# Optimization experiments

Hardware: AMD Instinct MI355X
Metric: run time of the kernel (lower is better)

The kernel has to match this reference:

```python
import jax, jax.numpy as jnp
import numpy as np
from math import sqrt

B, L, S, H, E = 4, 2048, 2048, 8, 64
T = 1.0  # softmax temperature


def setup_inputs() -> dict:
    key = jax.random.key(0)
    kq, kk, kv = jax.random.split(key, 3)
    q = jax.random.normal(kq, (B, L, H, E), dtype=jnp.float32)
    k = jax.random.normal(kk, (B, S, H, E), dtype=jnp.float32)
    v = jax.random.normal(kv, (B, S, H, E), dtype=jnp.float32)
    mask = jnp.zeros((B, L), dtype=jnp.bool_)  # unused by the module, kept for signature fidelity
    return {"q": q, "k": k, "v": v, "mask": mask}


def reference(q, k, v, mask):
    Bq, Lq, Hq, Eq = q.shape
    # [B,L,H,E] -> [B,H,E,L]; FFT over time axis
    xq = jnp.transpose(q, (0, 2, 3, 1))
    xk = jnp.transpose(k, (0, 2, 3, 1))
    xv = jnpp_t = jnp.transpose(v, (0, 2, 3, 1))
    xq_ft = jnp.fft.rfft(xq, axis=-1, norm='ortho')   # [B,H,E,Lf]
    xk_ft = jnp.fft.rfft(xk, axis=-1, norm='ortho')   # [B,H,E,Sf]
    xv_ft = jnp.fft.rfft(xv, axis=-1, norm='ortho')   # [B,H,E,Sf]
    # complex frequency-domain scores [B,H,Lf,Sf]
    scores = jnp.einsum('bhex,bhey->bhxy', xq_ft, jnp.conj(xk_ft)) / sqrt(Eq)
    # activation == 'softmax': softmax over |scores|/T, then real-weighted complex mix
    attn = jax.nn.softmax(jnp.abs(scores) / T, axis=-1)
    xqkv_ft = jnp.einsum('bhxy,bhey->bhex', attn.astype(xv_ft.dtype), xv_ft)  # [B,H,E,Lf]
    out = jnp.fft.irfft(xqkv_ft, n=Lq, axis=-1, norm='ortho')  # [B,H,E,L]
    return jnp.transpose(out, (0, 3, 1, 2))  # [B,L,H,E]
```

## Files before the change

kernel.cpp:

```cpp
#include <hip/hip_runtime.h>
#include <hip/hip_bf16.h>
#include <math.h>

#define LOGN  11
#define NN    2048
#define LOGM  10
#define MM    1024
#define NF    1025
#define NYP   1056
#define TWO_PI 6.283185307179586f
#define INV_SQRT_N 0.022097086912079608f
#define INV_SCALE  0.044194173824159216f

typedef __attribute__((ext_vector_type(8))) short bhalf8;
typedef __attribute__((ext_vector_type(4))) float f32x4;

#define MFMA16(a, b, c) __builtin_amdgcn_mfma_f32_16x16x32_bf16(a, b, c, 0, 0, 0)

__device__ __forceinline__ unsigned short f2bf(float f) {
    union { float f; unsigned u; } v; v.f = f;
    unsigned r = v.u + 0x7FFFu + ((v.u >> 16) & 1u);
    return (unsigned short)(r >> 16);
}
__device__ __forceinline__ float bf2f(unsigned short h) {
    union { unsigned u; float f; } v; v.u = ((unsigned)h) << 16;
    return v.f;
}

__device__ __forceinline__ void fft_stages_m(float2* buf, const float2* tw, int tid)
{
    for (int st = 1; st <= LOGM; st++) {
        int half = 1 << (st - 1);
        #pragma unroll
        for (int it = 0; it < 2; it++) {
            int j   = tid + 256 * it;
            int pos = j & (half - 1);
            int grp = j >> (st - 1);
            int i0  = (grp << st) + pos;
            int i1  = i0 + half;
            float2 w = tw[pos << (LOGM - st)];
            float2 a = buf[i0];
            float2 b = buf[i1];
            float2 bw = make_float2(b.x * w.x - b.y * w.y,
                                    b.x * w.y + b.y * w.x);
            buf[i0] = make_float2(a.x + bw.x, a.y + bw.y);
            buf[i1] = make_float2(a.x - bw.x, a.y - bw.y);
        }
        __syncthreads();
    }
}

__global__ __launch_bounds__(256) void tr_fwd(const float* __restrict__ q,
                                              const float* __restrict__ k,
                                              const float* __restrict__ v,
                                              unsigned short* __restrict__ ttr)
{
    __shared__ float Ts[64][65];
    int tt     = blockIdx.x;
    int h      = blockIdx.y;
    int z      = blockIdx.z;
    int tensor = z >> 2;
    int b      = z & 3;
    int tid    = threadIdx.x;
    int t0     = tt * 64;

    const float* in = (tensor == 0) ? q : (tensor == 1) ? k : v;

    {
        int tl = tid >> 2, ec = (tid & 3) * 16;
        const float* src = in + ((size_t)b * 2048 + t0 + tl) * 512 + h * 64 + ec;
        #pragma unroll
        for (int m = 0; m < 4; m++) {
            float4 v4 = *(const float4*)(src + m * 4);
            Ts[tl][ec + m * 4 + 0] = v4.x;
            Ts[tl][ec + m * 4 + 1] = v4.y;
            Ts[tl][ec + m * 4 + 2] = v4.z;
            Ts[tl][ec + m * 4 + 3] = v4.w;
        }
    }
    __syncthreads();
    {
        int el = tid >> 2, tc = (tid & 3) * 16;
        size_t row = ((size_t)(tensor * 32 + b * 8 + h)) * 64 + el;
        unsigned short* dst = ttr + row * 2048 + t0 + tc;
        #pragma unroll
        for (int j = 0; j < 16; j++) dst[j] = f2bf(Ts[tc + j][el]);
    }
}

__global__ __launch_bounds__(256) void fft_fwd(const unsigned short* __restrict__ ttr,
                                               unsigned short* __restrict__ Pq,
                                               unsigned short* __restrict__ Pk,
                                               unsigned short* __restrict__ Pv)
{
    __shared__ float2 buf[MM];
    __shared__ float2 tw[MM / 2];

    int g      = blockIdx.x;
    int p      = g % 96;
    int e      = g / 96;
    int tensor = p / 32;
    int bh     = p % 32;
    int tid    = threadIdx.x;

    unsigned short* plane = (tensor == 0) ? Pq : (tensor == 1) ? Pk : Pv;

    for (int i = tid; i < MM / 2; i += 256) {
        float ang = -TWO_PI * (float)i / (float)MM;
        float sv, cv;
        __sincosf(ang, &sv, &cv);
        tw[i] = make_float2(cv, sv);
    }

    const unsigned short* src = ttr + ((size_t)p * 64 + e) * 2048;
    #pragma unroll
    for (int i = 0; i < 4; i++) {
        int j = tid + 256 * i;
        unsigned pr = *(const unsigned*)(src + 2 * j);
        float x0 = bf2f((unsigned short)(pr & 0xFFFFu));
        float x1 = bf2f((unsigned short)(pr >> 16));
        buf[__brev((unsigned)j) >> (32 - LOGM)] = make_float2(x0, x1);
    }
    __syncthreads();

    fft_stages_m(buf, tw, tid);

    unsigned short* dre = plane + ((size_t)bh * 128 + e) * NYP;
    unsigned short* dim_ = dre + (size_t)64 * NYP;

    for (int kk = tid; kk < NF; kk += 256) {
        float2 A  = buf[kk & (MM - 1)];
        float2 Bc = buf[(MM - kk) & (MM - 1)];
        float Ex = 0.5f * (A.x + Bc.x), Ey = 0.5f * (A.y - Bc.y);
        float Dx = 0.5f * (A.x - Bc.x), Dy = 0.5f * (A.y + Bc.y);
        float Ox = Dy, Oy = -Dx;
        float th = -(TWO_PI / (float)NN) * (float)kk;
        float sn, cs;
        __sincosf(th, &sn, &cs);
        float Xr = Ex + cs * Ox - sn * Oy;
        float Xi = Ey + cs * Oy + sn * Ox;
        dre[kk]  = f2bf(Xr * INV_SQRT_N);
        dim_[kk] = f2bf(Xi * INV_SQRT_N);
    }
    for (int y = NF + tid; y < NYP; y += 256) { dre[y] = 0; dim_[y] = 0; }
}

__global__ __launch_bounds__(256) void qkpack(const unsigned short* __restrict__ Pq,
                                              const unsigned short* __restrict__ Pk,
                                              unsigned short* __restrict__ Qp,
                                              unsigned short* __restrict__ Kp)
{
    __shared__ unsigned short Ts[32][136];
    int y0  = blockIdx.x * 32;
    int bh  = blockIdx.y;
    int tsr = blockIdx.z;
    int tid = threadIdx.x;

    const unsigned short* srcp = (tsr == 0) ? Pq : Pk;
    unsigned short* dstp       = (tsr == 0) ? Qp : Kp;

    {
        int kk = tid >> 1, seg = tid & 1;
        const unsigned short* sp = srcp + ((size_t)bh * 128 + kk) * NYP + y0 + seg * 16;
        #pragma unroll
        for (int j = 0; j < 16; j++) Ts[seg * 16 + j][kk] = sp[j];
    }
    __syncthreads();
    {
        int y = tid >> 3, c = tid & 7;
        unsigned short* dst = dstp + ((size_t)bh * NYP + y0 + y) * 128 + c * 16;
        #pragma unroll
        for (int j = 0; j < 16; j++) dst[j] = Ts[y][c * 16 + j];
    }
}

struct FlashShared {
    union {
        struct {
            unsigned short Ks[32][136];
            unsigned short Vs[128][40];
        } kv;
        unsigned short OutT[128][72];
    } u;
    unsigned short Ps[4][16][40];
};

__global__ __launch_bounds__(256) void flash_mfma(
    const unsigned short* __restrict__ Qp,
    const unsigned short* __restrict__ Kp,
    const unsigned short* __restrict__ Vt,
    unsigned short* __restrict__ numb,
    float* __restrict__ lbuf)
{
    __shared__ FlashShared S;

    int g    = blockIdx.x;
    int bh   = g & 31;
    int idx  = g >> 5;
    int half = idx / 17;
    int x0   = (idx % 17) * 64;
    int tid  = threadIdx.x;
    int w    = tid >> 6;
    int lane = tid & 63;
    int qd   = lane >> 4;
    int col  = lane & 15;

    int xrow = x0 + w * 16 + col;
    int xq   = min(xrow, 1024);
    const unsigned short* qb = Qp + ((size_t)bh * NYP + xq) * 128 + qd * 8;
    bhalf8 Are[4], Aim[4];
    #pragma unroll
    for (int ks = 0; ks < 4; ks++) Are[ks] = *(const bhalf8*)(qb + ks * 32);
    Aim[0] = Are[2];
    Aim[1] = Are[3];
    #pragma unroll
    for (int ks = 0; ks < 2; ks++) {
        bhalf8 t = Are[ks];
        unsigned* u = (unsigned*)&t;
        #pragma unroll
        for (int j = 0; j < 4; j++) u[j] ^= 0x80008000u;
        Aim[ks + 2] = t;
    }

    f32x4 O[8];
    #pragma unroll
    for (int n = 0; n < 8; n++) O[n] = (f32x4){0.f, 0.f, 0.f, 0.f};
    float Lacc[4] = {0.f, 0.f, 0.f, 0.f};

    const unsigned short* kpb = Kp + (size_t)bh * NYP * 128;
    const unsigned short* vtb = Vt + (size_t)bh * 128 * NYP;

    int yy = tid >> 3, c = tid & 7;
    int ee = tid >> 1, h = tid & 1;

    int yt0 = half * 17, yt1 = min(33, yt0 + 17);

    uint4 kc0, kc1, vc0, vc1;
    {
        const uint4* s4 = (const uint4*)(kpb + ((size_t)(yt0 * 32 + yy)) * 128 + c * 16);
        kc0 = s4[0]; kc1 = s4[1];
        const uint4* s5 = (const uint4*)(vtb + (size_t)ee * NYP + yt0 * 32 + h * 16);
        vc0 = s5[0]; vc1 = s5[1];
    }

    for (int yt = yt0; yt < yt1; yt++) {
        __syncthreads();
        *(uint4*)&S.u.kv.Ks[yy][c * 16]     = kc0;
        *(uint4*)&S.u.kv.Ks[yy][c * 16 + 8] = kc1;
        *(uint4*)&S.u.kv.Vs[ee][h * 16]     = vc0;
        *(uint4*)&S.u.kv.Vs[ee][h * 16 + 8] = vc1;
        __syncthreads();

        uint4 kn0, kn1, vn0, vn1;
        if (yt + 1 < yt1) {
            int y0n = (yt + 1) * 32;
            const uint4* s4 = (const uint4*)(kpb + ((size_t)(y0n + yy)) * 128 + c * 16);
            kn0 = s4[0]; kn1 = s4[1];
            const uint4* s5 = (const uint4*)(vtb + (size_t)ee * NYP + y0n + h * 16);
            vn0 = s5[0]; vn1 = s5[1];
        }

        f32x4 sre[2], sim[2];
        #pragma unroll
        for (int sc = 0; sc < 2; sc++) {
            sre[sc] = (f32x4){0.f, 0.f, 0.f, 0.f};
            sim[sc] = (f32x4){0.f, 0.f, 0.f, 0.f};
        }
        #pragma unroll
        for (int sc = 0; sc < 2; sc++)
            #pragma unroll
            for (int ks = 0; ks < 4; ks++) {
                bhalf8 bfrag = *(const bhalf8*)&S.u.kv.Ks[col + 16 * sc][ks * 32 + qd * 8];
                sre[sc] = MFMA16(Are[ks], bfrag, sre[sc]);
                sim[sc] = MFMA16(Aim[ks], bfrag, sim[sc]);
            }

        #pragma unroll
        for (int r = 0; r < 4; r++) {
            float re0 = sre[0][r], im0 = sim[0][r];
            float re1 = sre[1][r], im1 = sim[1][r];
            float p0 = __expf(0.125f * sqrtf(re0 * re0 + im0 * im0));
            float p1 = __expf(0.125f * sqrtf(re1 * re1 + im1 * im1));
            Lacc[r] += p0 + p1;
            S.Ps[w][qd * 4 + r][col]      = f2bf(p0);
            S.Ps[w][qd * 4 + r][col + 16] = f2bf(p1);
        }

        bhalf8 pa = *(const bhalf8*)&S.Ps[w][col][qd * 8];
        #pragma unroll
        for (int n = 0; n < 8; n++) {
            bhalf8 bv = *(const bhalf8*)&S.u.kv.Vs[n * 16 + col][qd * 8];
            O[n] = MFMA16(pa, bv, O[n]);
        }

        kc0 = kn0; kc1 = kn1; vc0 = vn0; vc1 = vn1;
    }

    size_t hofs = (size_t)half * 32 * NYP;
    #pragma unroll
    for (int r = 0; r < 4; r++) {
        float ls = Lacc[r];
        ls += __shfl_xor(ls, 1);
        ls += __shfl_xor(ls, 2);
        ls += __shfl_xor(ls, 4);
        ls += __shfl_xor(ls, 8);
        if (half == 1) ls -= 31.0f;
        int x = x0 + w * 16 + qd * 4 + r;
        if (x <= 1024 && col == 0) lbuf[hofs + (size_t)bh * NYP + x] = ls;
    }

    __syncthreads();
    #pragma unroll
    for (int r = 0; r < 4; r++)
        #pragma unroll
        for (int n = 0; n < 8; n++)
            S.u.OutT[n * 16 + col][w * 16 + qd * 4 + r] = f2bf(O[n][r]);
    __syncthreads();
    {
        int kk2 = tid >> 1, seg = tid & 1;
        int xg  = x0 + seg * 32;
        if (xg < NYP) {
            unsigned short* dst =
                numb + (((size_t)half * 32 + bh) * 128 + kk2) * NYP + xg;
            const unsigned short* srcl = &S.u.OutT[kk2][seg * 32];
            #pragma unroll
            for (int m = 0; m < 4; m++)
                *(uint4*)(dst + m * 8) = *(const uint4*)(srcl + m * 8);
        }
    }
}

__global__ __launch_bounds__(256) void fft_inv(const unsigned short* __restrict__ numb,
                                               const float* __restrict__ lbuf,
                                               float* __restrict__ st)
{
    __shared__ float2 buf[MM];
    __shared__ float2 tw[MM / 2];

    int s   = blockIdx.x;
    int e   = s & 63;
    int bh  = s >> 6;
    int tid = threadIdx.x;

    for (int i = tid; i < MM / 2; i += 256) {
        float ang = TWO_PI * (float)i / (float)MM;
        float sv, cv;
        __sincosf(ang, &sv, &cv);
        tw[i] = make_float2(cv, sv);
    }

    const size_t HS = (size_t)32 * 128 * NYP;
    const unsigned short* nbr = numb + ((size_t)bh * 128 + e) * NYP;
    const unsigned short* nbi = numb + ((size_t)bh * 128 + 64 + e) * NYP;
    const float* l0 = lbuf + (size_t)bh * NYP;
    const float* l1 = l0 + (size_t)32 * NYP;

    #pragma unroll
    for (int i = 0; i < 4; i++) {
        int kk = tid + 256 * i;
        int x1 = kk, x2 = 1024 - kk;
        float iv1 = 1.f / (l0[x1] + l1[x1]);
        float iv2 = 1.f / (l0[x2] + l1[x2]);
        float Ax = (bf2f(nbr[x1]) + bf2f(nbr[HS + x1])) * iv1;
        float Ay = (bf2f(nbi[x1]) + bf2f(nbi[HS + x1])) * iv1;
        float Bx = (bf2f(nbr[x2]) + bf2f(nbr[HS + x2])) * iv2;
        float By = -((bf2f(nbi[x2]) + bf2f(nbi[HS + x2])) * iv2);
        float Ex = 0.5f * (Ax + Bx), Ey = 0.5f * (Ay + By);
        float Dx = 0.5f * (Ax - Bx), Dy = 0.5f * (Ay - By);
        float th = (TWO_PI / (float)NN) * (float)kk;
        float sn, cs;
        __sincosf(th, &sn, &cs);
        float Ox = Dx * cs - Dy * sn;
        float Oy = Dx * sn + Dy * cs;
        buf[__brev((unsigned)kk) >> (32 - LOGM)] = make_float2(Ex - Oy, Ey + Ox);
    }
    __syncthreads();

    fft_stages_m(buf, tw, tid);

    float* dst = st + ((size_t)bh * 64 + e) * 2048;
    #pragma unroll
    for (int i = 0; i < 4; i++) {
        int j = tid + 256 * i;
        float2 z = buf[j];
        *(float2*)&dst[2 * j] = make_float2(z.x * INV_SCALE, z.y * INV_SCALE);
    }
}

__global__ __launch_bounds__(256) void out_tr(const float* __restrict__ st,
                                              float* __restrict__ out)
{
    __shared__ float Ts[64][65];
    int tt  = blockIdx.x;
    int h   = blockIdx.y;
    int b   = blockIdx.z;
    int tid = threadIdx.x;
    int bh  = b * 8 + h;

    {
        int e = tid >> 2, tc = (tid & 3) * 16;
        const float* src = st + ((size_t)bh * 64 + e) * 2048 + tt * 64 + tc;
        #pragma unroll
        for (int m = 0; m < 4; m++) {
            float4 v4 = *(const float4*)(src + m * 4);
            Ts[e][tc + m * 4 + 0] = v4.x;
            Ts[e][tc + m * 4 + 1] = v4.y;
            Ts[e][tc + m * 4 + 2] = v4.z;
            Ts[e][tc + m * 4 + 3] = v4.w;
        }
    }
    __syncthreads();
    {
        int t = tid >> 2, ec = (tid & 3) * 16;
        float* dst = out + (size_t)b * 2048 * 512 + (size_t)(tt * 64 + t) * 512
                     + h * 64 + ec;
        #pragma unroll
        for (int m = 0; m < 4; m++) {
            float4 v4;
            v4.x = Ts[ec + m * 4 + 0][t];
            v4.y = Ts[ec + m * 4 + 1][t];
            v4.z = Ts[ec + m * 4 + 2][t];
            v4.w = Ts[ec + m * 4 + 3][t];
            *(float4*)(dst + m * 4) = v4;
        }
    }
}

extern "C" void kernel_launch(void* const* d_in, const int* in_sizes, int n_in,
                              void* d_out, int out_size, void* d_ws, size_t ws_size,
                              hipStream_t stream)
{
    const float* q = (const float*)d_in[0];
    const float* k = (const float*)d_in[1];
    const float* v = (const float*)d_in[2];
    float* out = (float*)d_out;

    char* ws = (char*)d_ws;
    const size_t PL = (size_t)32 * 128 * NYP * sizeof(unsigned short);
    unsigned short* Pq = (unsigned short*)(ws);
    unsigned short* Pk = (unsigned short*)(ws + PL);
    unsigned short* Pv = (unsigned short*)(ws + 2 * PL);
    unsigned short* ttr = (unsigned short*)(ws + 3 * PL);
    unsigned short* Qp = (unsigned short*)(ws + 3 * PL);
    unsigned short* Kp = (unsigned short*)(ws + 4 * PL);
    unsigned short* numb = (unsigned short*)(ws);
    float* st   = (float*)(ws + 3 * PL);
    float* lbuf = (float*)(ws + 5 * PL);

    hipLaunchKernelGGL(tr_fwd, dim3(32, 8, 12), dim3(256), 0, stream,
                       q, k, v, ttr);
    hipLaunchKernelGGL(fft_fwd, dim3(3 * 2048), dim3(256), 0, stream,
                       ttr, Pq, Pk, Pv);
    hipLaunchKernelGGL(qkpack, dim3(33, 32, 2), dim3(256), 0, stream,
                       Pq, Pk, Qp, Kp);
    hipLaunchKernelGGL(flash_mfma, dim3(1088), dim3(256), 0, stream,
                       Qp, Kp, Pv, numb, lbuf);
    hipLaunchKernelGGL(fft_inv, dim3(2048), dim3(256), 0, stream,
                       numb, lbuf, st);
    hipLaunchKernelGGL(out_tr, dim3(32, 8, 4), dim3(256), 0, stream,
                       st, out);
}
```

Baseline: 233.0 us.

## Use two waves per flash block, each handling 32 query rows

The flash attention kernel now runs 128 threads (2 waves) per block instead of 4, and each wave processes two 16-row query sub-tiles. Each K and V fragment read from LDS now feeds twice as many MFMAs, which cuts LDS reads and staging work per unit of compute. The cost is roughly double the accumulator and Q-fragment registers per wave, and fewer waves per block to hide latency, which could lower occupancy.

```diff
diff --git a/kernel.cpp b/kernel.cpp
--- a/kernel.cpp
+++ b/kernel.cpp
@@ -182,10 +182,10 @@
         } kv;
         unsigned short OutT[128][72];
     } u;
-    unsigned short Ps[4][16][40];
+    unsigned short Ps[2][32][40];
 };
 
-__global__ __launch_bounds__(256) void flash_mfma(
+__global__ __launch_bounds__(128) void flash_mfma(
     const unsigned short* __restrict__ Qp,
     const unsigned short* __restrict__ Kp,
     const unsigned short* __restrict__ Vt,
@@ -205,127 +205,148 @@
     int qd   = lane >> 4;
     int col  = lane & 15;
 
-    int xrow = x0 + w * 16 + col;
-    int xq   = min(xrow, 1024);
-    const unsigned short* qb = Qp + ((size_t)bh * NYP + xq) * 128 + qd * 8;
-    bhalf8 Are[4], Aim[4];
-    #pragma unroll
-    for (int ks = 0; ks < 4; ks++) Are[ks] = *(const bhalf8*)(qb + ks * 32);
-    Aim[0] = Are[2];
-    Aim[1] = Are[3];
-    #pragma unroll
-    for (int ks = 0; ks < 2; ks++) {
-        bhalf8 t = Are[ks];
-        unsigned* u = (unsigned*)&t;
-        #pragma unroll
-        for (int j = 0; j < 4; j++) u[j] ^= 0x80008000u;
-        Aim[ks + 2] = t;
-    }
-
-    f32x4 O[8];
-    #pragma unroll
-    for (int n = 0; n < 8; n++) O[n] = (f32x4){0.f, 0.f, 0.f, 0.f};
-    float Lacc[4] = {0.f, 0.f, 0.f, 0.f};
+    bhalf8 Are[2][4];
+    bhalf8 Aneg[2][2];
+    #pragma unroll
+    for (int s = 0; s < 2; s++) {
+        int xq = min(x0 + w * 32 + s * 16 + col, 1024);
+        const unsigned short* qb = Qp + ((size_t)bh * NYP + xq) * 128 + qd * 8;
+        #pragma unroll
+        for (int ks = 0; ks < 4; ks++) Are[s][ks] = *(const bhalf8*)(qb + ks * 32);
+        #pragma unroll
+        for (int ks = 0; ks < 2; ks++) {
+            bhalf8 t = Are[s][ks];
+            unsigned* u = (unsigned*)&t;
+            #pragma unroll
+            for (int j = 0; j < 4; j++) u[j] ^= 0x80008000u;
+            Aneg[s][ks] = t;
+        }
+    }
+
+    f32x4 O[2][8];
+    #pragma unroll
+    for (int s = 0; s < 2; s++)
+        #pragma unroll
+        for (int n = 0; n < 8; n++) O[s][n] = (f32x4){0.f, 0.f, 0.f, 0.f};
+    float Lacc[2][4] = {{0.f, 0.f, 0.f, 0.f}, {0.f, 0.f, 0.f, 0.f}};
 
     const unsigned short* kpb = Kp + (size_t)bh * NYP * 128;
     const unsigned short* vtb = Vt + (size_t)bh * 128 * NYP;
 
-    int yy = tid >> 3, c = tid & 7;
-    int ee = tid >> 1, h = tid & 1;
+    int krow[4], vrow[4];
+    #pragma unroll
+    for (int m = 0; m < 4; m++) {
+        krow[m] = (m * 128 + tid) >> 4;
+        vrow[m] = (m * 128 + tid) >> 2;
+    }
+    int kcol = (tid & 15) * 8, vcol = (tid & 3) * 8;
 
     int yt0 = half * 17, yt1 = min(33, yt0 + 17);
 
-    uint4 kc0, kc1, vc0, vc1;
-    {
-        const uint4* s4 = (const uint4*)(kpb + ((size_t)(yt0 * 32 + yy)) * 128 + c * 16);
-        kc0 = s4[0]; kc1 = s4[1];
-        const uint4* s5 = (const uint4*)(vtb + (size_t)ee * NYP + yt0 * 32 + h * 16);
-        vc0 = s5[0]; vc1 = s5[1];
+    uint4 kc[4], vc[4];
+    #pragma unroll
+    for (int m = 0; m < 4; m++) {
+        kc[m] = *(const uint4*)(kpb + ((size_t)(yt0 * 32 + krow[m])) * 128 + kcol);
+        vc[m] = *(const uint4*)(vtb + (size_t)vrow[m] * NYP + yt0 * 32 + vcol);
     }
 
     for (int yt = yt0; yt < yt1; yt++) {
         __syncthreads();
-        *(uint4*)&S.u.kv.Ks[yy][c * 16]     = kc0;
-        *(uint4*)&S.u.kv.Ks[yy][c * 16 + 8] = kc1;
-        *(uint4*)&S.u.kv.Vs[ee][h * 16]     = vc0;
-        *(uint4*)&S.u.kv.Vs[ee][h * 16 + 8] = vc1;
+        #pragma unroll
+        for (int m = 0; m < 4; m++) {
+            *(uint4*)&S.u.kv.Ks[krow[m]][kcol] = kc[m];
+            *(uint4*)&S.u.kv.Vs[vrow[m]][vcol] = vc[m];
+        }
         __syncthreads();
 
-        uint4 kn0, kn1, vn0, vn1;
         if (yt + 1 < yt1) {
             int y0n = (yt + 1) * 32;
-            const uint4* s4 = (const uint4*)(kpb + ((size_t)(y0n + yy)) * 128 + c * 16);
-            kn0 = s4[0]; kn1 = s4[1];
-            const uint4* s5 = (const uint4*)(vtb + (size_t)ee * NYP + y0n + h * 16);
-            vn0 = s5[0]; vn1 = s5[1];
-        }
-
-        f32x4 sre[2], sim[2];
-        #pragma unroll
-        for (int sc = 0; sc < 2; sc++) {
-            sre[sc] = (f32x4){0.f, 0.f, 0.f, 0.f};
-            sim[sc] = (f32x4){0.f, 0.f, 0.f, 0.f};
-        }
+            #pragma unroll
+            for (int m = 0; m < 4; m++) {
+                kc[m] = *(const uint4*)(kpb + ((size_t)(y0n + krow[m])) * 128 + kcol);
+                vc[m] = *(const uint4*)(vtb + (size_t)vrow[m] * NYP + y0n + vcol);
+            }
+        }
+
+        f32x4 sre[2][2], sim[2][2];
+        #pragma unroll
+        for (int s = 0; s < 2; s++)
+            #pragma unroll
+            for (int sc = 0; sc < 2; sc++) {
+                sre[s][sc] = (f32x4){0.f, 0.f, 0.f, 0.f};
+                sim[s][sc] = (f32x4){0.f, 0.f, 0.f, 0.f};
+            }
         #pragma unroll
         for (int sc = 0; sc < 2; sc++)
             #pragma unroll
             for (int ks = 0; ks < 4; ks++) {
                 bhalf8 bfrag = *(const bhalf8*)&S.u.kv.Ks[col + 16 * sc][ks * 32 + qd * 8];
-                sre[sc] = MFMA16(Are[ks], bfrag, sre[sc]);
-                sim[sc] = MFMA16(Aim[ks], bfrag, sim[sc]);
+                #pragma unroll
+                for (int s = 0; s < 2; s++) {
+                    sre[s][sc] = MFMA16(Are[s][ks], bfrag, sre[s][sc]);
+                    bhalf8 ai = (ks < 2) ? Are[s][ks + 2] : Aneg[s][ks - 2];
+                    sim[s][sc] = MFMA16(ai, bfrag, sim[s][sc]);
+                }
             }
 
         #pragma unroll
-        for (int r = 0; r < 4; r++) {
-            float re0 = sre[0][r], im0 = sim[0][r];
-            float re1 = sre[1][r], im1 = sim[1][r];
-            float p0 = __expf(0.125f * sqrtf(re0 * re0 + im0 * im0));
-            float p1 = __expf(0.125f * sqrtf(re1 * re1 + im1 * im1));
-            Lacc[r] += p0 + p1;
-            S.Ps[w][qd * 4 + r][col]      = f2bf(p0);
-            S.Ps[w][qd * 4 + r][col + 16] = f2bf(p1);
-        }
-
-        bhalf8 pa = *(const bhalf8*)&S.Ps[w][col][qd * 8];
+        for (int s = 0; s < 2; s++)
+            #pragma unroll
+            for (int r = 0; r < 4; r++) {
+                float re0 = sre[s][0][r], im0 = sim[s][0][r];
+                float re1 = sre[s][1][r], im1 = sim[s][1][r];
+                float p0 = __expf(0.125f * sqrtf(re0 * re0 + im0 * im0));
+                float p1 = __expf(0.125f * sqrtf(re1 * re1 + im1 * im1));
+                Lacc[s][r] += p0 + p1;
+                S.Ps[w][s * 16 + qd * 4 + r][col]      = f2bf(p0);
+                S.Ps[w][s * 16 + qd * 4 + r][col + 16] = f2bf(p1);
+            }
+
+        bhalf8 pa0 = *(const bhalf8*)&S.Ps[w][col][qd * 8];
+        bhalf8 pa1 = *(const bhalf8*)&S.Ps[w][16 + col][qd * 8];
         #pragma unroll
         for (int n = 0; n < 8; n++) {
             bhalf8 bv = *(const bhalf8*)&S.u.kv.Vs[n * 16 + col][qd * 8];
-            O[n] = MFMA16(pa, bv, O[n]);
-        }
-
-        kc0 = kn0; kc1 = kn1; vc0 = vn0; vc1 = vn1;
+            O[0][n] = MFMA16(pa0, bv, O[0][n]);
+            O[1][n] = MFMA16(pa1, bv, O[1][n]);
+        }
     }
 
     size_t hofs = (size_t)half * 32 * NYP;
     #pragma unroll
-    for (int r = 0; r < 4; r++) {
-        float ls = Lacc[r];
-        ls += __shfl_xor(ls, 1);
-        ls += __shfl_xor(ls, 2);
-        ls += __shfl_xor(ls, 4);
-        ls += __shfl_xor(ls, 8);
-        if (half == 1) ls -= 31.0f;
-        int x = x0 + w * 16 + qd * 4 + r;
-        if (x <= 1024 && col == 0) lbuf[hofs + (size_t)bh * NYP + x] = ls;
-    }
-
-    __syncthreads();
-    #pragma unroll
-    for (int r = 0; r < 4; r++)
-        #pragma unroll
-        for (int n = 0; n < 8; n++)
-            S.u.OutT[n * 16 + col][w * 16 + qd * 4 + r] = f2bf(O[n][r]);
-    __syncthreads();
-    {
-        int kk2 = tid >> 1, seg = tid & 1;
-        int xg  = x0 + seg * 32;
-        if (xg < NYP) {
-            unsigned short* dst =
-                numb + (((size_t)half * 32 + bh) * 128 + kk2) * NYP + xg;
-            const unsigned short* srcl = &S.u.OutT[kk2][seg * 32];
-            #pragma unroll
-            for (int m = 0; m < 4; m++)
-                *(uint4*)(dst + m * 8) = *(const uint4*)(srcl + m * 8);
+    for (int s = 0; s < 2; s++)
+        #pragma unroll
+        for (int r = 0; r < 4; r++) {
+            float ls = Lacc[s][r];
+            ls += __shfl_xor(ls, 1);
+            ls += __shfl_xor(ls, 2);
+            ls += __shfl_xor(ls, 4);
+            ls += __shfl_xor(ls, 8);
+            if (half == 1) ls -= 31.0f;
+            int x = x0 + w * 32 + s * 16 + qd * 4 + r;
+            if (x <= 1024 && col == 0) lbuf[hofs + (size_t)bh * NYP + x] = ls;
+        }
+
+    __syncthreads();
+    #pragma unroll
+    for (int s = 0; s < 2; s++)
+        #pragma unroll
+        for (int r = 0; r < 4; r++)
+            #pragma unroll
+            for (int n = 0; n < 8; n++)
+                S.u.OutT[n * 16 + col][w * 32 + s * 16 + qd * 4 + r] = f2bf(O[s][n][r]);
+    __syncthreads();
+    {
+        int kk2 = tid;
+        unsigned short* dst =
+            numb + (((size_t)half * 32 + bh) * 128 + kk2) * NYP + x0;
+        #pragma unroll
+        for (int seg = 0; seg < 4; seg++) {
+            int cx = seg * 16;
+            if (x0 + cx < NYP) {
+                *(uint4*)(dst + cx)     = *(const uint4*)&S.u.OutT[kk2][cx];
+                *(uint4*)(dst + cx + 8) = *(const uint4*)&S.u.OutT[kk2][cx + 8];
+            }
         }
     }
 }
@@ -453,7 +474,7 @@
                        ttr, Pq, Pk, Pv);
     hipLaunchKernelGGL(qkpack, dim3(33, 32, 2), dim3(256), 0, stream,
                        Pq, Pk, Qp, Kp);
-    hipLaunchKernelGGL(flash_mfma, dim3(1088), dim3(256), 0, stream,
+    hipLaunchKernelGGL(flash_mfma, dim3(1088), dim3(128), 0, stream,
                        Qp, Kp, Pv, numb, lbuf);
     hipLaunchKernelGGL(fft_inv, dim3(2048), dim3(256), 0, stream,
                        numb, lbuf, st);
```

After: 294.9 us. 26.6% more time.
